# Kernel tuning notes

Hardware: AMD Instinct MI355X
Metric: run time of the kernel (lower is better)

The kernel has to match this reference:

```python
import jax, jax.numpy as jnp
import numpy as np

B, S, D, H = 2, 2048, 1024, 16
DEPTH = D // H

def setup_inputs() -> dict:
    key = jax.random.key(0)
    ks = jax.random.split(key, 6)
    sc = 0.02
    return {
        "x": jax.random.normal(ks[0], (B, S, D), dtype=jnp.float32),
        "mask": jnp.ones((S, S), dtype=jnp.int32),
        "wq": jax.random.normal(ks[1], (D, D), dtype=jnp.float32) * sc,
        "bq": jnp.zeros((D,), dtype=jnp.float32),
        "wk": jax.random.normal(ks[2], (D, D), dtype=jnp.float32) * sc,
        "bk": jnp.zeros((D,), dtype=jnp.float32),
        "wv": jax.random.normal(ks[3], (D, D), dtype=jnp.float32) * sc,
        "bv": jnp.zeros((D,), dtype=jnp.float32),
        "wo": jax.random.normal(ks[4], (D, D), dtype=jnp.float32) * sc,
        "bo": jnp.zeros((D,), dtype=jnp.float32),
    }

def _split_heads(t):
    # [B,S,D] -> [B,H,S,depth]
    b, s, _ = t.shape
    return t.reshape(b, s, H, DEPTH).transpose(0, 2, 1, 3)

def reference(x, mask, wq, bq, wk, bk, wv, bv, wo, bo):
    q = _split_heads(x @ wq + bq)
    k = _split_heads(x @ wk + bk)
    v = _split_heads(x @ wv + bv)
    scale = 1.0 / jnp.sqrt(jnp.asarray(DEPTH, x.dtype))
    scores = jnp.einsum('bhqd,bhkd->bhqk', q, k) * scale
    # Faithful to original: band_part(ones,-1,0) is the LOWER triangle
    # (incl. diagonal), and it is ADDED times -1e9 -> lower triangle masked.
    s_len = mask.shape[0]
    tri = jnp.tril(jnp.ones((s_len, s_len), dtype=x.dtype))
    scores = scores + tri * (-1e9)
    attn = jax.nn.softmax(scores, axis=-1)  # dropout is identity at inference
    out = jnp.einsum('bhqk,bhkd->bhqd', attn, v)
    out = out.transpose(0, 2, 1, 3).reshape(x.shape[0], -1, D)
    return out @ wo + bo
```

## Files before the change

### kernel.cpp

```cpp
#include <hip/hip_runtime.h>
#include <hip/hip_bf16.h>


using bf16   = __bf16;
using bf16x2 = __attribute__((ext_vector_type(2))) __bf16;
using bf16x4 = __attribute__((ext_vector_type(4))) __bf16;
using bf16x8 = __attribute__((ext_vector_type(8))) __bf16;
using f32x4  = __attribute__((ext_vector_type(4))) float;
using uintx2 = __attribute__((ext_vector_type(2))) unsigned int;
using uintx4 = __attribute__((ext_vector_type(4))) unsigned int;

__device__ __forceinline__ void load_lds16(const void* g, void* l) {
  __builtin_amdgcn_global_load_lds(
      (const __attribute__((address_space(1))) void*)g,
      (__attribute__((address_space(3))) void*)l, 16, 0, 0);
}

__device__ __forceinline__ unsigned int packbf(float a, float b) {
  bf16x2 v;
  v[0] = (bf16)a;
  v[1] = (bf16)b;
  return __builtin_bit_cast(unsigned int, v);
}

__device__ __forceinline__ void xchg_p(unsigned int u, unsigned int v, int hi,
                                       unsigned int& f, unsigned int& s) {
#if __has_builtin(__builtin_amdgcn_permlane32_swap) && \
    __has_builtin(__builtin_amdgcn_permlane16_swap)
  uintx2 ab = __builtin_amdgcn_permlane32_swap(u, v, false, false);
  uintx2 fs = __builtin_amdgcn_permlane16_swap(ab[0], ab[1], false, false);
  f = fs[0];
  s = fs[1];
#else
  unsigned int a = (hi < 2) ? u : (unsigned int)__shfl_xor((int)v, 32);
  unsigned int b = (hi < 2) ? (unsigned int)__shfl_xor((int)u, 32) : v;
  unsigned int a16 = (unsigned int)__shfl_xor((int)a, 16);
  unsigned int b16 = (unsigned int)__shfl_xor((int)b, 16);
  f = (hi & 1) ? b16 : a;
  s = (hi & 1) ? b : a16;
#endif
}

__global__ __launch_bounds__(256) void prep_kernel(
    const float* __restrict__ x, bf16* __restrict__ xb,
    const float* __restrict__ wq, const float* __restrict__ wk,
    const float* __restrict__ wv, const float* __restrict__ wo,
    bf16* __restrict__ wT) {
  const int t = threadIdx.x;
  int bid = blockIdx.x;
  if (bid < 4096) {
    const int i = (bid * 256 + t) * 4;
    const float4 v = *(const float4*)(x + i);
    bf16x4 o;
    o[0] = (bf16)v.x; o[1] = (bf16)v.y; o[2] = (bf16)v.z; o[3] = (bf16)v.w;
    *(bf16x4*)(xb + i) = o;
    return;
  }
  bid -= 4096;
  const int sel = bid >> 8;
  const float* w = (sel == 0) ? wq : (sel == 1) ? wk : (sel == 2) ? wv : wo;
  bf16* out = wT + (size_t)sel * 1048576;
  __shared__ float tile[64][65];
  const int n0 = (bid & 15) * 64;
  const int k0 = ((bid >> 4) & 15) * 64;
#pragma unroll
  for (int p = 0; p < 4; ++p) {
    const int row = p * 16 + (t >> 4);
    const int c4  = (t & 15) * 4;
    const float4 v = *(const float4*)&w[(size_t)(k0 + row) * 1024 + n0 + c4];
    tile[row][c4 + 0] = v.x; tile[row][c4 + 1] = v.y;
    tile[row][c4 + 2] = v.z; tile[row][c4 + 3] = v.w;
  }
  __syncthreads();
#pragma unroll
  for (int p = 0; p < 4; ++p) {
    const int rn = p * 16 + (t >> 4);
    const int c4 = (t & 15) * 4;
    bf16x4 o;
#pragma unroll
    for (int j = 0; j < 4; ++j) o[j] = (bf16)tile[c4 + j][rn];
    *(bf16x4*)&out[(size_t)(n0 + rn) * 1024 + k0 + c4] = o;
  }
}

template <int MODE>
__global__ __launch_bounds__(256, 2) void gemm_bt(
    const bf16* __restrict__ A, const bf16* __restrict__ Bt,
    const float* __restrict__ bias0, const float* __restrict__ bias1,
    const float* __restrict__ bias2, bf16* __restrict__ qf,
    bf16* __restrict__ kf, bf16* __restrict__ vt, float* __restrict__ fout,
    int Nblocks) {
  __shared__ __align__(16) char smem[32768];
  char* sA = smem;
  char* sB = smem + 16384;
  const int tid = threadIdx.x;
  const int lane = tid & 63;
  const int w = tid >> 6;
  const int wm = w >> 1, wn = w & 1;
  const int bid = blockIdx.x;
  const int m0 = (bid / Nblocks) * 128;
  const int n0 = (bid % Nblocks) * 128;

  const char* Ab = (const char*)A;
  const char* Bb = (const char*)Bt;
  size_t srcA[4], srcB[4];
#pragma unroll
  for (int it = 0; it < 4; ++it) {
    const int o = it * 4096 + tid * 16;
    const int r = o >> 7;
    const int cg = ((o >> 4) & 7) ^ (r & 7);
    srcA[it] = (size_t)(m0 + r) * 2048 + cg * 16;
    srcB[it] = (size_t)(n0 + r) * 2048 + cg * 16;
  }

  f32x4 acc[4][4] = {};

  for (int kt = 0; kt < 16; ++kt) {
    const size_t kb = (size_t)kt * 128;
#pragma unroll
    for (int it = 0; it < 4; ++it) {
      load_lds16(Ab + srcA[it] + kb, sA + it * 4096 + w * 1024);
      load_lds16(Bb + srcB[it] + kb, sB + it * 4096 + w * 1024);
    }
    asm volatile("s_waitcnt vmcnt(0)" ::: "memory");
    __syncthreads();
#pragma unroll
    for (int ks = 0; ks < 2; ++ks) {
      bf16x8 aF[4], bF[4];
      const int g = (lane >> 4) + 4 * ks;
#pragma unroll
      for (int i = 0; i < 4; ++i) {
        const int ra = wm * 64 + i * 16 + (lane & 15);
        aF[i] = *(const bf16x8*)(sA + ra * 128 + ((g ^ (ra & 7)) << 4));
        const int rb = wn * 64 + i * 16 + (lane & 15);
        bF[i] = *(const bf16x8*)(sB + rb * 128 + ((g ^ (rb & 7)) << 4));
      }
#pragma unroll
      for (int mi = 0; mi < 4; ++mi)
#pragma unroll
        for (int ni = 0; ni < 4; ++ni)
          acc[mi][ni] = __builtin_amdgcn_mfma_f32_16x16x32_bf16(
              aF[mi], bF[ni], acc[mi][ni], 0, 0, 0);
    }
    __syncthreads();
  }

  const int cn = lane & 15;
  const int gq = lane >> 4;
#pragma unroll
  for (int mi = 0; mi < 4; ++mi) {
#pragma unroll
    for (int ni = 0; ni < 4; ++ni) {
      const int n  = n0 + wn * 64 + ni * 16 + cn;
      const int mb = m0 + wm * 64 + mi * 16 + 4 * gq;
      const f32x4 v = acc[mi][ni];
      if (MODE == 0) {
        const float bias =
            (n < 1024) ? bias0[n] : ((n < 2048) ? bias1[n - 1024] : bias2[n - 2048]);
        if (n < 2048) {
          bf16* dst = (n < 1024) ? qf : kf;
          const int nn = n & 1023;
#pragma unroll
          for (int j = 0; j < 4; ++j)
            dst[(size_t)(mb + j) * 1024 + nn] = (bf16)(v[j] + bias);
        } else {
          const int nn = n - 2048;
          const int hh = nn >> 6, dd = nn & 63;
          const int bb = mb >> 11, ss = mb & 2047;
          bf16x4 pk;
#pragma unroll
          for (int j = 0; j < 4; ++j) pk[j] = (bf16)(v[j] + bias);
          *(bf16x4*)(vt + ((size_t)((bb * 16 + hh) * 64 + dd) * 2048 + ss)) = pk;
        }
      } else {
        const float bias = bias0[n];
#pragma unroll
        for (int j = 0; j < 4; ++j)
          fout[(size_t)(mb + j) * 1024 + n] = v[j] + bias;
      }
    }
  }
}

__global__ __launch_bounds__(256, 3) void attn_kernel(
    const bf16* __restrict__ qf, const bf16* __restrict__ kf,
    const bf16* __restrict__ vt, bf16* __restrict__ ao,
    bf16* __restrict__ o2buf, float* __restrict__ mlbuf) {
  __shared__ __align__(16) char smem[32768];

  const unsigned int TAB[24] = {
      0u | (0u << 8)  | (16u << 16) | (1u << 24),
      0u | (16u << 8) | (32u << 16) | (2u << 24),
      1u | (2u << 8)  | (17u << 16) | (1u << 24),
      1u | (17u << 8) | (32u << 16) | (2u << 24),
      2u | (4u << 8)  | (18u << 16) | (1u << 24),
      2u | (18u << 8) | (32u << 16) | (2u << 24),
      3u | (6u << 8)  | (19u << 16) | (1u << 24),
      4u | (8u << 8)  | (20u << 16) | (1u << 24),
      8u | (16u << 8) | (32u << 16) | (0u << 24),
      9u | (18u << 8) | (32u << 16) | (0u << 24),
      3u | (19u << 8) | (32u << 16) | (2u << 24),
      5u | (10u << 8) | (21u << 16) | (1u << 24),
      5u | (21u << 8) | (32u << 16) | (2u << 24),
      6u | (12u << 8) | (22u << 16) | (1u << 24),
      4u | (20u << 8) | (32u << 16) | (2u << 24),
      10u | (20u << 8) | (32u << 16) | (0u << 24),
      15u | (30u << 8) | (32u << 16) | (0u << 24),
      14u | (28u << 8) | (32u << 16) | (0u << 24),
      13u | (26u << 8) | (32u << 16) | (0u << 24),
      12u | (24u << 8) | (32u << 16) | (0u << 24),
      7u | (14u << 8) | (23u << 16) | (1u << 24),
      6u | (22u << 8) | (32u << 16) | (2u << 24),
      7u | (23u << 8) | (32u << 16) | (2u << 24),
      11u | (22u << 8) | (32u << 16) | (0u << 24)};

  const int tid  = threadIdx.x;
  const int lane = tid & 63;
  const int hi   = lane >> 4;
  const int qlo  = lane & 15;
  const int w    = tid >> 6;
  const int u  = blockIdx.x >> 5;
  const int bh = blockIdx.x & 31;
  const int b = bh >> 4, h = bh & 15;
  const unsigned int ent = TAB[u];
  const int jq = ent & 255, kbeg = (ent >> 8) & 255, kend = (ent >> 16) & 255;
  const int mode = ent >> 24;

  const char* kbase = (const char*)kf + ((size_t)b * 2048) * 2048 + h * 128;
  const char* vbase = (const char*)vt + (size_t)bh * 262144;
  const char* qbb   = (const char*)qf + ((size_t)b * 2048) * 2048 + h * 128;

  const int sr  = tid >> 3;
  const int scg = (tid & 7) ^ (sr & 7);

  bf16x8 onesB;
#pragma unroll
  for (int i = 0; i < 8; ++i) onesB[i] = (bf16)1.0f;

  const int q0 = jq * 128;
  const int qb = q0 + w * 32;

  bf16x8 qA[2][2];
#pragma unroll
  for (int nt = 0; nt < 2; ++nt) {
    const char* qrow = qbb + (size_t)(qb + 16 * nt + qlo) * 2048;
#pragma unroll
    for (int ks = 0; ks < 2; ++ks) {
      qA[nt][ks] = *(const bf16x8*)(qrow + ks * 64 + hi * 16);
#pragma unroll
      for (int i = 0; i < 8; ++i)
        qA[nt][ks][i] = (bf16)(0.125f * (float)qA[nt][ks][i]);
    }
  }

  float m[2] = {-1e30f, -1e30f};
  f32x4 lacc[2] = {};
  f32x4 O[2][4] = {};

  auto STAGE = [&](int kt, int bufi) {
    char* dK = smem + bufi * 8192 + w * 1024;
    char* dV = smem + 16384 + bufi * 8192 + w * 1024;
    const int kn = kt * 64;
#pragma unroll
    for (int p = 0; p < 2; ++p) {
      load_lds16(kbase + (size_t)(kn + sr + 32 * p) * 2048 + scg * 16,
                 dK + p * 4096);
      load_lds16(vbase + (size_t)(sr + 32 * p) * 4096 + (size_t)kn * 2 +
                     scg * 16,
                 dV + p * 4096);
    }
  };

  STAGE(kbeg, 0);
  __syncthreads();

  for (int kt = kbeg; kt < kend; ++kt) {
    const int cur = (kt - kbeg) & 1;

    if (kt + 1 < kend) STAGE(kt + 1, cur ^ 1);

    const char* bK = smem + cur * 8192;
    const char* bV = smem + 16384 + cur * 8192;

    f32x4 sc[2][4] = {};
#pragma unroll
    for (int ks = 0; ks < 2; ++ks) {
      const int g = hi + 4 * ks;
#pragma unroll
      for (int t = 0; t < 4; ++t) {
        const int rk = t * 16 + qlo;
        const bf16x8 kF =
            *(const bf16x8*)(bK + rk * 128 + ((g ^ (rk & 7)) << 4));
        sc[0][t] = __builtin_amdgcn_mfma_f32_16x16x32_bf16(kF, qA[0][ks],
                                                           sc[0][t], 0, 0, 0);
        sc[1][t] = __builtin_amdgcn_mfma_f32_16x16x32_bf16(kF, qA[1][ks],
                                                           sc[1][t], 0, 0, 0);
      }
    }

    if (kt * 64 < q0 + 128) {
      const int k0t = kt * 64;
#pragma unroll
      for (int nt = 0; nt < 2; ++nt)
#pragma unroll
        for (int t = 0; t < 4; ++t)
#pragma unroll
          for (int j = 0; j < 4; ++j) {
            const int kk = k0t + t * 16 + 4 * hi + j;
            const int qq = qb + 16 * nt + qlo;
            if (kk <= qq) sc[nt][t][j] = -1e30f;
          }
    }

    float tm[2];
#pragma unroll
    for (int nt = 0; nt < 2; ++nt) {
      float v = sc[nt][0][0];
#pragma unroll
      for (int t = 0; t < 4; ++t)
#pragma unroll
        for (int j = 0; j < 4; ++j) v = fmaxf(v, sc[nt][t][j]);
      v = fmaxf(v, __shfl_xor(v, 16));
      v = fmaxf(v, __shfl_xor(v, 32));
      tm[nt] = v;
    }

    const bool grew = (tm[0] - m[0] > 8.0f) || (tm[1] - m[1] > 8.0f);
    if (__any(grew)) {
#pragma unroll
      for (int nt = 0; nt < 2; ++nt) {
        const float mn = fmaxf(m[nt], tm[nt]);
        const float al = __expf(m[nt] - mn);
        m[nt] = mn;
#pragma unroll
        for (int j = 0; j < 4; ++j) {
          const float alj = __shfl(al, 4 * hi + j);
          lacc[nt][j] *= alj;
#pragma unroll
          for (int dt = 0; dt < 4; ++dt) O[nt][dt][j] *= alj;
        }
      }
    }

    bf16x8 pA[2][2];
#pragma unroll
    for (int nt = 0; nt < 2; ++nt) {
      unsigned int W[4][2];
#pragma unroll
      for (int t = 0; t < 4; ++t)
#pragma unroll
        for (int p = 0; p < 2; ++p)
          W[t][p] = packbf(__expf(sc[nt][t][2 * p] - m[nt]),
                           __expf(sc[nt][t][2 * p + 1] - m[nt]));
#pragma unroll
      for (int ks = 0; ks < 2; ++ks) {
        uintx4 w4;
#pragma unroll
        for (int p = 0; p < 2; ++p) {
          unsigned int f, s;
          xchg_p(W[2 * ks][p], W[2 * ks + 1][p], hi, f, s);
          w4[p] = f;
          w4[2 + p] = s;
        }
        pA[nt][ks] = __builtin_bit_cast(bf16x8, w4);
        lacc[nt] = __builtin_amdgcn_mfma_f32_16x16x32_bf16(pA[nt][ks], onesB,
                                                           lacc[nt], 0, 0, 0);
      }
    }

#pragma unroll
    for (int ks = 0; ks < 2; ++ks) {
      const int g = hi + 4 * ks;
#pragma unroll
      for (int dt = 0; dt < 4; ++dt) {
        const int rv = dt * 16 + qlo;
        const bf16x8 vF =
            *(const bf16x8*)(bV + rv * 128 + ((g ^ (rv & 7)) << 4));
        O[0][dt] = __builtin_amdgcn_mfma_f32_16x16x32_bf16(pA[0][ks], vF,
                                                           O[0][dt], 0, 0, 0);
        O[1][dt] = __builtin_amdgcn_mfma_f32_16x16x32_bf16(pA[1][ks], vF,
                                                           O[1][dt], 0, 0, 0);
      }
    }
    __syncthreads();
  }

  if (mode == 0) {
#pragma unroll
    for (int nt = 0; nt < 2; ++nt)
#pragma unroll
      for (int j = 0; j < 4; ++j) {
        const float linv = (lacc[nt][j] > 0.f) ? 1.f / lacc[nt][j] : 0.f;
        const int qg = qb + 16 * nt + 4 * hi + j;
#pragma unroll
        for (int dt = 0; dt < 4; ++dt)
          ao[(size_t)(b * 2048 + qg) * 1024 + h * 64 + dt * 16 + qlo] =
              (bf16)(O[nt][dt][j] * linv);
      }
  } else {
    const int qtbh = jq * 32 + bh;
    const int slot = mode - 1;
#pragma unroll
    for (int nt = 0; nt < 2; ++nt)
#pragma unroll
      for (int j = 0; j < 4; ++j) {
        const int r = w * 32 + 16 * nt + 4 * hi + j;
#pragma unroll
        for (int dt = 0; dt < 4; ++dt) {
          const bf16 vv = (bf16)O[nt][dt][j];
          if (mode == 1)
            ao[(size_t)(b * 2048 + q0 + r) * 1024 + h * 64 + dt * 16 + qlo] = vv;
          else
            o2buf[(size_t)(qtbh * 128 + r) * 64 + dt * 16 + qlo] = vv;
        }
      }
    if (qlo == 0) {
#pragma unroll
      for (int nt = 0; nt < 2; ++nt)
#pragma unroll
        for (int j = 0; j < 4; ++j)
          mlbuf[((qtbh * 2 + slot) * 2 + 1) * 128 + (w * 32 + 16 * nt + 4 * hi + j)] =
              lacc[nt][j];
    }
    if (hi == 0) {
#pragma unroll
      for (int nt = 0; nt < 2; ++nt)
        mlbuf[((qtbh * 2 + slot) * 2 + 0) * 128 + (w * 32 + 16 * nt + qlo)] =
            m[nt];
    }
  }
}

__global__ __launch_bounds__(256) void combine_kernel(
    const bf16* __restrict__ o2buf, const float* __restrict__ mlbuf,
    bf16* __restrict__ ao) {
  const int qtbh = blockIdx.x;
  const int jq = qtbh >> 5, bh = qtbh & 31;
  const int b = bh >> 4, h = bh & 15;
  const int t = threadIdx.x;
  const int r = t >> 1;
  const int c0 = (t & 1) * 32;

  const float m1 = mlbuf[((qtbh * 2 + 0) * 2 + 0) * 128 + r];
  const float l1 = mlbuf[((qtbh * 2 + 0) * 2 + 1) * 128 + r];
  const float m2 = mlbuf[((qtbh * 2 + 1) * 2 + 0) * 128 + r];
  const float l2 = mlbuf[((qtbh * 2 + 1) * 2 + 1) * 128 + r];
  const float M  = fmaxf(m1, m2);
  const float w1 = __expf(m1 - M), w2 = __expf(m2 - M);
  const float denom = w1 * l1 + w2 * l2;
  const float linv = (denom > 0.f) ? 1.f / denom : 0.f;

  bf16* arow = ao + ((size_t)(b * 2048 + jq * 128 + r) * 1024 + h * 64 + c0);
  const bf16* o2row = o2buf + ((size_t)(qtbh * 128 + r) * 64 + c0);
#pragma unroll
  for (int i = 0; i < 4; ++i) {
    const bf16x8 o1 = *(const bf16x8*)(arow + i * 8);
    const bf16x8 o2 = *(const bf16x8*)(o2row + i * 8);
    bf16x8 o;
#pragma unroll
    for (int j = 0; j < 8; ++j)
      o[j] = (bf16)((w1 * (float)o1[j] + w2 * (float)o2[j]) * linv);
    *(bf16x8*)(arow + i * 8) = o;
  }
}

__global__ __launch_bounds__(256) void vmean_kernel(const bf16* __restrict__ vt,
                                                    bf16* __restrict__ ao) {
  const int tid = threadIdx.x;
  const int lane = tid & 63, w = tid >> 6;
  const int gw = blockIdx.x * 4 + w;
  const int bh = gw >> 6, d = gw & 63;
  const int b = bh >> 4, h = bh & 15;
  const bf16x8* p = (const bf16x8*)(vt + (size_t)gw * 2048 + lane * 32);
  float s = 0.f;
#pragma unroll
  for (int i = 0; i < 4; ++i) {
    const bf16x8 v = p[i];
#pragma unroll
    for (int j = 0; j < 8; ++j) s += (float)v[j];
  }
  for (int off = 1; off < 64; off <<= 1) s += __shfl_xor(s, off);
  if (lane == 0)
    ao[(size_t)(b * 2048 + 2047) * 1024 + h * 64 + d] = (bf16)(s * (1.f / 2048.f));
}

extern "C" void kernel_launch(void* const* d_in, const int* in_sizes, int n_in,
                              void* d_out, int out_size, void* d_ws,
                              size_t ws_size, hipStream_t stream) {
  const float* x  = (const float*)d_in[0];
  const float* wq = (const float*)d_in[2];
  const float* bq = (const float*)d_in[3];
  const float* wk = (const float*)d_in[4];
  const float* bk = (const float*)d_in[5];
  const float* wv = (const float*)d_in[6];
  const float* bv = (const float*)d_in[7];
  const float* wo = (const float*)d_in[8];
  const float* bo = (const float*)d_in[9];
  float* out = (float*)d_out;

  if (ws_size < (size_t)25165824 * 2) return;

  bf16* ws    = (bf16*)d_ws;
  bf16* xb    = ws;
  bf16* wqkvT = xb + 4194304;
  bf16* woT   = wqkvT + 3145728;
  bf16* qfp   = woT + 1048576;
  bf16* kfp   = qfp + 4194304;
  bf16* vtp   = kfp + 4194304;
  bf16* aop   = vtp + 4194304;

  bf16*  o2buf = xb;
  float* mlbuf = (float*)(xb + 2097152);

  prep_kernel<<<5120, 256, 0, stream>>>(x, xb, wq, wk, wv, wo, wqkvT);

  gemm_bt<0><<<32 * 24, 256, 0, stream>>>(xb, wqkvT, bq, bk, bv, qfp, kfp, vtp,
                                          nullptr, 24);
  attn_kernel<<<768, 256, 0, stream>>>(qfp, kfp, vtp, aop, o2buf, mlbuf);
  vmean_kernel<<<512, 256, 0, stream>>>(vtp, aop);
  combine_kernel<<<256, 256, 0, stream>>>(o2buf, mlbuf, aop);
  gemm_bt<1><<<32 * 8, 256, 0, stream>>>(aop, woT, bo, nullptr, nullptr, nullptr,
                                         nullptr, nullptr, out, 8);
}
```

Baseline: 106.9 us.

## Make attention kernel persistent with atomic work-queue scheduling

The attention kernel becomes persistent: 512 blocks repeatedly take work units from a global atomic counter that prep_kernel resets, and the unit table moves to device constant memory in a new order. The goal is to balance the uneven causal-split work across CUs dynamically instead of relying on the hardware's static block dispatch. Launch bounds drop from 3 to 2 waves per EU to match the persistent grid. This adds one atomic plus a block barrier per unit and uses fewer resident blocks, so some latency hiding may be lost.

```diff
diff --git a/kernel.cpp b/kernel.cpp
--- a/kernel.cpp
+++ b/kernel.cpp
@@ -9,6 +9,32 @@
 using f32x4  = __attribute__((ext_vector_type(4))) float;
 using uintx2 = __attribute__((ext_vector_type(2))) unsigned int;
 using uintx4 = __attribute__((ext_vector_type(4))) unsigned int;
+
+__device__ const unsigned int kUnitTab[24] = {
+    0u | (0u << 8)  | (16u << 16) | (1u << 24),
+    0u | (16u << 8) | (32u << 16) | (2u << 24),
+    8u | (16u << 8) | (32u << 16) | (0u << 24),
+    1u | (2u << 8)  | (17u << 16) | (1u << 24),
+    1u | (17u << 8) | (32u << 16) | (2u << 24),
+    2u | (4u << 8)  | (18u << 16) | (1u << 24),
+    2u | (18u << 8) | (32u << 16) | (2u << 24),
+    9u | (18u << 8) | (32u << 16) | (0u << 24),
+    3u | (6u << 8)  | (19u << 16) | (1u << 24),
+    3u | (19u << 8) | (32u << 16) | (2u << 24),
+    4u | (8u << 8)  | (20u << 16) | (1u << 24),
+    4u | (20u << 8) | (32u << 16) | (2u << 24),
+    10u | (20u << 8) | (32u << 16) | (0u << 24),
+    5u | (10u << 8) | (21u << 16) | (1u << 24),
+    5u | (21u << 8) | (32u << 16) | (2u << 24),
+    6u | (12u << 8) | (22u << 16) | (1u << 24),
+    6u | (22u << 8) | (32u << 16) | (2u << 24),
+    11u | (22u << 8) | (32u << 16) | (0u << 24),
+    7u | (14u << 8) | (23u << 16) | (1u << 24),
+    7u | (23u << 8) | (32u << 16) | (2u << 24),
+    12u | (24u << 8) | (32u << 16) | (0u << 24),
+    13u | (26u << 8) | (32u << 16) | (0u << 24),
+    14u | (28u << 8) | (32u << 16) | (0u << 24),
+    15u | (30u << 8) | (32u << 16) | (0u << 24)};
 
 __device__ __forceinline__ void load_lds16(const void* g, void* l) {
   __builtin_amdgcn_global_load_lds(
@@ -45,9 +71,10 @@
     const float* __restrict__ x, bf16* __restrict__ xb,
     const float* __restrict__ wq, const float* __restrict__ wk,
     const float* __restrict__ wv, const float* __restrict__ wo,
-    bf16* __restrict__ wT) {
+    bf16* __restrict__ wT, int* __restrict__ ctr) {
   const int t = threadIdx.x;
   int bid = blockIdx.x;
+  if (bid == 0 && t == 0) *ctr = 0;
   if (bid < 4096) {
     const int i = (bid * 256 + t) * 4;
     const float4 v = *(const float4*)(x + i);
@@ -182,53 +209,19 @@
   }
 }
 
-__global__ __launch_bounds__(256, 3) void attn_kernel(
+__global__ __launch_bounds__(256, 2) void attn_kernel(
     const bf16* __restrict__ qf, const bf16* __restrict__ kf,
     const bf16* __restrict__ vt, bf16* __restrict__ ao,
-    bf16* __restrict__ o2buf, float* __restrict__ mlbuf) {
+    bf16* __restrict__ o2buf, float* __restrict__ mlbuf,
+    int* __restrict__ ctr) {
   __shared__ __align__(16) char smem[32768];
-
-  const unsigned int TAB[24] = {
-      0u | (0u << 8)  | (16u << 16) | (1u << 24),
-      0u | (16u << 8) | (32u << 16) | (2u << 24),
-      1u | (2u << 8)  | (17u << 16) | (1u << 24),
-      1u | (17u << 8) | (32u << 16) | (2u << 24),
-      2u | (4u << 8)  | (18u << 16) | (1u << 24),
-      2u | (18u << 8) | (32u << 16) | (2u << 24),
-      3u | (6u << 8)  | (19u << 16) | (1u << 24),
-      4u | (8u << 8)  | (20u << 16) | (1u << 24),
-      8u | (16u << 8) | (32u << 16) | (0u << 24),
-      9u | (18u << 8) | (32u << 16) | (0u << 24),
-      3u | (19u << 8) | (32u << 16) | (2u << 24),
-      5u | (10u << 8) | (21u << 16) | (1u << 24),
-      5u | (21u << 8) | (32u << 16) | (2u << 24),
-      6u | (12u << 8) | (22u << 16) | (1u << 24),
-      4u | (20u << 8) | (32u << 16) | (2u << 24),
-      10u | (20u << 8) | (32u << 16) | (0u << 24),
-      15u | (30u << 8) | (32u << 16) | (0u << 24),
-      14u | (28u << 8) | (32u << 16) | (0u << 24),
-      13u | (26u << 8) | (32u << 16) | (0u << 24),
-      12u | (24u << 8) | (32u << 16) | (0u << 24),
-      7u | (14u << 8) | (23u << 16) | (1u << 24),
-      6u | (22u << 8) | (32u << 16) | (2u << 24),
-      7u | (23u << 8) | (32u << 16) | (2u << 24),
-      11u | (22u << 8) | (32u << 16) | (0u << 24)};
+  __shared__ int s_g;
 
   const int tid  = threadIdx.x;
   const int lane = tid & 63;
   const int hi   = lane >> 4;
   const int qlo  = lane & 15;
   const int w    = tid >> 6;
-  const int u  = blockIdx.x >> 5;
-  const int bh = blockIdx.x & 31;
-  const int b = bh >> 4, h = bh & 15;
-  const unsigned int ent = TAB[u];
-  const int jq = ent & 255, kbeg = (ent >> 8) & 255, kend = (ent >> 16) & 255;
-  const int mode = ent >> 24;
-
-  const char* kbase = (const char*)kf + ((size_t)b * 2048) * 2048 + h * 128;
-  const char* vbase = (const char*)vt + (size_t)bh * 262144;
-  const char* qbb   = (const char*)qf + ((size_t)b * 2048) * 2048 + h * 128;
 
   const int sr  = tid >> 3;
   const int scg = (tid & 7) ^ (sr & 7);
@@ -237,196 +230,215 @@
 #pragma unroll
   for (int i = 0; i < 8; ++i) onesB[i] = (bf16)1.0f;
 
-  const int q0 = jq * 128;
-  const int qb = q0 + w * 32;
-
-  bf16x8 qA[2][2];
-#pragma unroll
-  for (int nt = 0; nt < 2; ++nt) {
-    const char* qrow = qbb + (size_t)(qb + 16 * nt + qlo) * 2048;
-#pragma unroll
-    for (int ks = 0; ks < 2; ++ks) {
-      qA[nt][ks] = *(const bf16x8*)(qrow + ks * 64 + hi * 16);
-#pragma unroll
-      for (int i = 0; i < 8; ++i)
-        qA[nt][ks][i] = (bf16)(0.125f * (float)qA[nt][ks][i]);
+  for (;;) {
+    if (tid == 0) s_g = atomicAdd(ctr, 1);
+    __syncthreads();
+    const int g = s_g;
+    if (g >= 768) break;
+
+    const unsigned int ent = kUnitTab[g >> 5];
+    const int bh = g & 31;
+    const int b = bh >> 4, h = bh & 15;
+    const int jq = ent & 255, kbeg = (ent >> 8) & 255,
+              kend = (ent >> 16) & 255;
+    const int mode = ent >> 24;
+
+    const char* kbase = (const char*)kf + ((size_t)b * 2048) * 2048 + h * 128;
+    const char* vbase = (const char*)vt + (size_t)bh * 262144;
+    const char* qbb   = (const char*)qf + ((size_t)b * 2048) * 2048 + h * 128;
+
+    const int q0 = jq * 128;
+    const int qb = q0 + w * 32;
+
+    bf16x8 qA[2][2];
+#pragma unroll
+    for (int nt = 0; nt < 2; ++nt) {
+      const char* qrow = qbb + (size_t)(qb + 16 * nt + qlo) * 2048;
+#pragma unroll
+      for (int ks = 0; ks < 2; ++ks) {
+        qA[nt][ks] = *(const bf16x8*)(qrow + ks * 64 + hi * 16);
+#pragma unroll
+        for (int i = 0; i < 8; ++i)
+          qA[nt][ks][i] = (bf16)(0.125f * (float)qA[nt][ks][i]);
+      }
     }
-  }
-
-  float m[2] = {-1e30f, -1e30f};
-  f32x4 lacc[2] = {};
-  f32x4 O[2][4] = {};
-
-  auto STAGE = [&](int kt, int bufi) {
-    char* dK = smem + bufi * 8192 + w * 1024;
-    char* dV = smem + 16384 + bufi * 8192 + w * 1024;
-    const int kn = kt * 64;
-#pragma unroll
-    for (int p = 0; p < 2; ++p) {
-      load_lds16(kbase + (size_t)(kn + sr + 32 * p) * 2048 + scg * 16,
-                 dK + p * 4096);
-      load_lds16(vbase + (size_t)(sr + 32 * p) * 4096 + (size_t)kn * 2 +
-                     scg * 16,
-                 dV + p * 4096);
+
+    float m[2] = {-1e30f, -1e30f};
+    f32x4 lacc[2] = {};
+    f32x4 O[2][4] = {};
+
+    auto STAGE = [&](int kt, int bufi) {
+      char* dK = smem + bufi * 8192 + w * 1024;
+      char* dV = smem + 16384 + bufi * 8192 + w * 1024;
+      const int kn = kt * 64;
+#pragma unroll
+      for (int p = 0; p < 2; ++p) {
+        load_lds16(kbase + (size_t)(kn + sr + 32 * p) * 2048 + scg * 16,
+                   dK + p * 4096);
+        load_lds16(vbase + (size_t)(sr + 32 * p) * 4096 + (size_t)kn * 2 +
+                       scg * 16,
+                   dV + p * 4096);
+      }
+    };
+
+    STAGE(kbeg, 0);
+    __syncthreads();
+
+    for (int kt = kbeg; kt < kend; ++kt) {
+      const int cur = (kt - kbeg) & 1;
+
+      if (kt + 1 < kend) STAGE(kt + 1, cur ^ 1);
+
+      const char* bK = smem + cur * 8192;
+      const char* bV = smem + 16384 + cur * 8192;
+
+      f32x4 sc[2][4] = {};
+#pragma unroll
+      for (int ks = 0; ks < 2; ++ks) {
+        const int gg = hi + 4 * ks;
+#pragma unroll
+        for (int t = 0; t < 4; ++t) {
+          const int rk = t * 16 + qlo;
+          const bf16x8 kF =
+              *(const bf16x8*)(bK + rk * 128 + ((gg ^ (rk & 7)) << 4));
+          sc[0][t] = __builtin_amdgcn_mfma_f32_16x16x32_bf16(kF, qA[0][ks],
+                                                             sc[0][t], 0, 0, 0);
+          sc[1][t] = __builtin_amdgcn_mfma_f32_16x16x32_bf16(kF, qA[1][ks],
+                                                             sc[1][t], 0, 0, 0);
+        }
+      }
+
+      if (kt * 64 < q0 + 128) {
+        const int k0t = kt * 64;
+#pragma unroll
+        for (int nt = 0; nt < 2; ++nt)
+#pragma unroll
+          for (int t = 0; t < 4; ++t)
+#pragma unroll
+            for (int j = 0; j < 4; ++j) {
+              const int kk = k0t + t * 16 + 4 * hi + j;
+              const int qq = qb + 16 * nt + qlo;
+              if (kk <= qq) sc[nt][t][j] = -1e30f;
+            }
+      }
+
+      float tm[2];
+#pragma unroll
+      for (int nt = 0; nt < 2; ++nt) {
+        float v = sc[nt][0][0];
+#pragma unroll
+        for (int t = 0; t < 4; ++t)
+#pragma unroll
+          for (int j = 0; j < 4; ++j) v = fmaxf(v, sc[nt][t][j]);
+        v = fmaxf(v, __shfl_xor(v, 16));
+        v = fmaxf(v, __shfl_xor(v, 32));
+        tm[nt] = v;
+      }
+
+      const bool grew = (tm[0] - m[0] > 8.0f) || (tm[1] - m[1] > 8.0f);
+      if (__any(grew)) {
+#pragma unroll
+        for (int nt = 0; nt < 2; ++nt) {
+          const float mn = fmaxf(m[nt], tm[nt]);
+          const float al = __expf(m[nt] - mn);
+          m[nt] = mn;
+#pragma unroll
+          for (int j = 0; j < 4; ++j) {
+            const float alj = __shfl(al, 4 * hi + j);
+            lacc[nt][j] *= alj;
+#pragma unroll
+            for (int dt = 0; dt < 4; ++dt) O[nt][dt][j] *= alj;
+          }
+        }
+      }
+
+      bf16x8 pA[2][2];
+#pragma unroll
+      for (int nt = 0; nt < 2; ++nt) {
+        unsigned int W[4][2];
+#pragma unroll
+        for (int t = 0; t < 4; ++t)
+#pragma unroll
+          for (int p = 0; p < 2; ++p)
+            W[t][p] = packbf(__expf(sc[nt][t][2 * p] - m[nt]),
+                             __expf(sc[nt][t][2 * p + 1] - m[nt]));
+#pragma unroll
+        for (int ks = 0; ks < 2; ++ks) {
+          uintx4 w4;
+#pragma unroll
+          for (int p = 0; p < 2; ++p) {
+            unsigned int f, s;
+            xchg_p(W[2 * ks][p], W[2 * ks + 1][p], hi, f, s);
+            w4[p] = f;
+            w4[2 + p] = s;
+          }
+          pA[nt][ks] = __builtin_bit_cast(bf16x8, w4);
+          lacc[nt] = __builtin_amdgcn_mfma_f32_16x16x32_bf16(pA[nt][ks], onesB,
+                                                             lacc[nt], 0, 0, 0);
+        }
+      }
+
+#pragma unroll
+      for (int ks = 0; ks < 2; ++ks) {
+        const int gg = hi + 4 * ks;
+#pragma unroll
+        for (int dt = 0; dt < 4; ++dt) {
+          const int rv = dt * 16 + qlo;
+          const bf16x8 vF =
+              *(const bf16x8*)(bV + rv * 128 + ((gg ^ (rv & 7)) << 4));
+          O[0][dt] = __builtin_amdgcn_mfma_f32_16x16x32_bf16(pA[0][ks], vF,
+                                                             O[0][dt], 0, 0, 0);
+          O[1][dt] = __builtin_amdgcn_mfma_f32_16x16x32_bf16(pA[1][ks], vF,
+                                                             O[1][dt], 0, 0, 0);
+        }
+      }
+      __syncthreads();
     }
-  };
-
-  STAGE(kbeg, 0);
-  __syncthreads();
-
-  for (int kt = kbeg; kt < kend; ++kt) {
-    const int cur = (kt - kbeg) & 1;
-
-    if (kt + 1 < kend) STAGE(kt + 1, cur ^ 1);
-
-    const char* bK = smem + cur * 8192;
-    const char* bV = smem + 16384 + cur * 8192;
-
-    f32x4 sc[2][4] = {};
-#pragma unroll
-    for (int ks = 0; ks < 2; ++ks) {
-      const int g = hi + 4 * ks;
-#pragma unroll
-      for (int t = 0; t < 4; ++t) {
-        const int rk = t * 16 + qlo;
-        const bf16x8 kF =
-            *(const bf16x8*)(bK + rk * 128 + ((g ^ (rk & 7)) << 4));
-        sc[0][t] = __builtin_amdgcn_mfma_f32_16x16x32_bf16(kF, qA[0][ks],
-                                                           sc[0][t], 0, 0, 0);
-        sc[1][t] = __builtin_amdgcn_mfma_f32_16x16x32_bf16(kF, qA[1][ks],
-                                                           sc[1][t], 0, 0, 0);
-      }
-    }
-
-    if (kt * 64 < q0 + 128) {
-      const int k0t = kt * 64;
+
+    if (mode == 0) {
 #pragma unroll
       for (int nt = 0; nt < 2; ++nt)
 #pragma unroll
-        for (int t = 0; t < 4; ++t)
-#pragma unroll
-          for (int j = 0; j < 4; ++j) {
-            const int kk = k0t + t * 16 + 4 * hi + j;
-            const int qq = qb + 16 * nt + qlo;
-            if (kk <= qq) sc[nt][t][j] = -1e30f;
+        for (int j = 0; j < 4; ++j) {
+          const float linv = (lacc[nt][j] > 0.f) ? 1.f / lacc[nt][j] : 0.f;
+          const int qg = qb + 16 * nt + 4 * hi + j;
+#pragma unroll
+          for (int dt = 0; dt < 4; ++dt)
+            ao[(size_t)(b * 2048 + qg) * 1024 + h * 64 + dt * 16 + qlo] =
+                (bf16)(O[nt][dt][j] * linv);
+        }
+    } else {
+      const int qtbh = jq * 32 + bh;
+      const int slot = mode - 1;
+#pragma unroll
+      for (int nt = 0; nt < 2; ++nt)
+#pragma unroll
+        for (int j = 0; j < 4; ++j) {
+          const int r = w * 32 + 16 * nt + 4 * hi + j;
+#pragma unroll
+          for (int dt = 0; dt < 4; ++dt) {
+            const bf16 vv = (bf16)O[nt][dt][j];
+            if (mode == 1)
+              ao[(size_t)(b * 2048 + q0 + r) * 1024 + h * 64 + dt * 16 + qlo] =
+                  vv;
+            else
+              o2buf[(size_t)(qtbh * 128 + r) * 64 + dt * 16 + qlo] = vv;
           }
-    }
-
-    float tm[2];
-#pragma unroll
-    for (int nt = 0; nt < 2; ++nt) {
-      float v = sc[nt][0][0];
-#pragma unroll
-      for (int t = 0; t < 4; ++t)
-#pragma unroll
-        for (int j = 0; j < 4; ++j) v = fmaxf(v, sc[nt][t][j]);
-      v = fmaxf(v, __shfl_xor(v, 16));
-      v = fmaxf(v, __shfl_xor(v, 32));
-      tm[nt] = v;
-    }
-
-    const bool grew = (tm[0] - m[0] > 8.0f) || (tm[1] - m[1] > 8.0f);
-    if (__any(grew)) {
-#pragma unroll
-      for (int nt = 0; nt < 2; ++nt) {
-        const float mn = fmaxf(m[nt], tm[nt]);
-        const float al = __expf(m[nt] - mn);
-        m[nt] = mn;
-#pragma unroll
-        for (int j = 0; j < 4; ++j) {
-          const float alj = __shfl(al, 4 * hi + j);
-          lacc[nt][j] *= alj;
-#pragma unroll
-          for (int dt = 0; dt < 4; ++dt) O[nt][dt][j] *= alj;
-        }
-      }
-    }
-
-    bf16x8 pA[2][2];
-#pragma unroll
-    for (int nt = 0; nt < 2; ++nt) {
-      unsigned int W[4][2];
-#pragma unroll
-      for (int t = 0; t < 4; ++t)
-#pragma unroll
-        for (int p = 0; p < 2; ++p)
-          W[t][p] = packbf(__expf(sc[nt][t][2 * p] - m[nt]),
-                           __expf(sc[nt][t][2 * p + 1] - m[nt]));
-#pragma unroll
-      for (int ks = 0; ks < 2; ++ks) {
-        uintx4 w4;
-#pragma unroll
-        for (int p = 0; p < 2; ++p) {
-          unsigned int f, s;
-          xchg_p(W[2 * ks][p], W[2 * ks + 1][p], hi, f, s);
-          w4[p] = f;
-          w4[2 + p] = s;
-        }
-        pA[nt][ks] = __builtin_bit_cast(bf16x8, w4);
-        lacc[nt] = __builtin_amdgcn_mfma_f32_16x16x32_bf16(pA[nt][ks], onesB,
-                                                           lacc[nt], 0, 0, 0);
-      }
-    }
-
-#pragma unroll
-    for (int ks = 0; ks < 2; ++ks) {
-      const int g = hi + 4 * ks;
-#pragma unroll
-      for (int dt = 0; dt < 4; ++dt) {
-        const int rv = dt * 16 + qlo;
-        const bf16x8 vF =
-            *(const bf16x8*)(bV + rv * 128 + ((g ^ (rv & 7)) << 4));
-        O[0][dt] = __builtin_amdgcn_mfma_f32_16x16x32_bf16(pA[0][ks], vF,
-                                                           O[0][dt], 0, 0, 0);
-        O[1][dt] = __builtin_amdgcn_mfma_f32_16x16x32_bf16(pA[1][ks], vF,
-                                                           O[1][dt], 0, 0, 0);
-      }
-    }
-    __syncthreads();
-  }
-
-  if (mode == 0) {
-#pragma unroll
-    for (int nt = 0; nt < 2; ++nt)
-#pragma unroll
-      for (int j = 0; j < 4; ++j) {
-        const float linv = (lacc[nt][j] > 0.f) ? 1.f / lacc[nt][j] : 0.f;
-        const int qg = qb + 16 * nt + 4 * hi + j;
-#pragma unroll
-        for (int dt = 0; dt < 4; ++dt)
-          ao[(size_t)(b * 2048 + qg) * 1024 + h * 64 + dt * 16 + qlo] =
-              (bf16)(O[nt][dt][j] * linv);
-      }
-  } else {
-    const int qtbh = jq * 32 + bh;
-    const int slot = mode - 1;
-#pragma unroll
-    for (int nt = 0; nt < 2; ++nt)
-#pragma unroll
-      for (int j = 0; j < 4; ++j) {
-        const int r = w * 32 + 16 * nt + 4 * hi + j;
-#pragma unroll
-        for (int dt = 0; dt < 4; ++dt) {
-          const bf16 vv = (bf16)O[nt][dt][j];
-          if (mode == 1)
-            ao[(size_t)(b * 2048 + q0 + r) * 1024 + h * 64 + dt * 16 + qlo] = vv;
-          else
-            o2buf[(size_t)(qtbh * 128 + r) * 64 + dt * 16 + qlo] = vv;
-        }
-      }
-    if (qlo == 0) {
-#pragma unroll
-      for (int nt = 0; nt < 2; ++nt)
-#pragma unroll
-        for (int j = 0; j < 4; ++j)
-          mlbuf[((qtbh * 2 + slot) * 2 + 1) * 128 + (w * 32 + 16 * nt + 4 * hi + j)] =
-              lacc[nt][j];
-    }
-    if (hi == 0) {
-#pragma unroll
-      for (int nt = 0; nt < 2; ++nt)
-        mlbuf[((qtbh * 2 + slot) * 2 + 0) * 128 + (w * 32 + 16 * nt + qlo)] =
-            m[nt];
+        }
+      if (qlo == 0) {
+#pragma unroll
+        for (int nt = 0; nt < 2; ++nt)
+#pragma unroll
+          for (int j = 0; j < 4; ++j)
+            mlbuf[((qtbh * 2 + slot) * 2 + 1) * 128 +
+                  (w * 32 + 16 * nt + 4 * hi + j)] = lacc[nt][j];
+      }
+      if (hi == 0) {
+#pragma unroll
+        for (int nt = 0; nt < 2; ++nt)
+          mlbuf[((qtbh * 2 + slot) * 2 + 0) * 128 + (w * 32 + 16 * nt + qlo)] =
+              m[nt];
+      }
     }
   }
 }
@@ -498,7 +510,7 @@
   const float* bo = (const float*)d_in[9];
   float* out = (float*)d_out;
 
-  if (ws_size < (size_t)25165824 * 2) return;
+  if (ws_size < (size_t)25165824 * 2 + 64) return;
 
   bf16* ws    = (bf16*)d_ws;
   bf16* xb    = ws;
@@ -508,15 +520,16 @@
   bf16* kfp   = qfp + 4194304;
   bf16* vtp   = kfp + 4194304;
   bf16* aop   = vtp + 4194304;
+  int*  ctr   = (int*)(aop + 4194304);
 
   bf16*  o2buf = xb;
   float* mlbuf = (float*)(xb + 2097152);
 
-  prep_kernel<<<5120, 256, 0, stream>>>(x, xb, wq, wk, wv, wo, wqkvT);
+  prep_kernel<<<5120, 256, 0, stream>>>(x, xb, wq, wk, wv, wo, wqkvT, ctr);
 
   gemm_bt<0><<<32 * 24, 256, 0, stream>>>(xb, wqkvT, bq, bk, bv, qfp, kfp, vtp,
                                           nullptr, 24);
-  attn_kernel<<<768, 256, 0, stream>>>(qfp, kfp, vtp, aop, o2buf, mlbuf);
+  attn_kernel<<<512, 256, 0, stream>>>(qfp, kfp, vtp, aop, o2buf, mlbuf, ctr);
   vmean_kernel<<<512, 256, 0, stream>>>(vtp, aop);
   combine_kernel<<<256, 256, 0, stream>>>(o2buf, mlbuf, aop);
   gemm_bt<1><<<32 * 8, 256, 0, stream>>>(aop, woT, bo, nullptr, nullptr, nullptr,
```

After: 121.1 us. +13.3%, slower.

## Pair causal attention segments per block to balance work across 512 blocks

Applied to the files above, without the earlier changes.

Replaces the 24-entry work table with a computed schedule. Blocks 0-7 each handle one long first-half segment. Blocks 8-15 each run two segments back to back, pairing query tile j's tail with query tile 15-j so every block covers about 15-16 key tiles. The grid shrinks from 768 to 512 blocks and the launch-bounds occupancy hint drops from 3 to 2. The aim is evenly sized blocks in a single wave, cutting tail imbalance and per-block launch overhead, at the cost of less parallelism and a serial second segment that reloads Q and restarts the pipeline.

```diff
diff --git a/kernel.cpp b/kernel.cpp
--- a/kernel.cpp
+++ b/kernel.cpp
@@ -182,37 +182,11 @@
   }
 }
 
-__global__ __launch_bounds__(256, 3) void attn_kernel(
+__global__ __launch_bounds__(256, 2) void attn_kernel(
     const bf16* __restrict__ qf, const bf16* __restrict__ kf,
     const bf16* __restrict__ vt, bf16* __restrict__ ao,
     bf16* __restrict__ o2buf, float* __restrict__ mlbuf) {
   __shared__ __align__(16) char smem[32768];
-
-  const unsigned int TAB[24] = {
-      0u | (0u << 8)  | (16u << 16) | (1u << 24),
-      0u | (16u << 8) | (32u << 16) | (2u << 24),
-      1u | (2u << 8)  | (17u << 16) | (1u << 24),
-      1u | (17u << 8) | (32u << 16) | (2u << 24),
-      2u | (4u << 8)  | (18u << 16) | (1u << 24),
-      2u | (18u << 8) | (32u << 16) | (2u << 24),
-      3u | (6u << 8)  | (19u << 16) | (1u << 24),
-      4u | (8u << 8)  | (20u << 16) | (1u << 24),
-      8u | (16u << 8) | (32u << 16) | (0u << 24),
-      9u | (18u << 8) | (32u << 16) | (0u << 24),
-      3u | (19u << 8) | (32u << 16) | (2u << 24),
-      5u | (10u << 8) | (21u << 16) | (1u << 24),
-      5u | (21u << 8) | (32u << 16) | (2u << 24),
-      6u | (12u << 8) | (22u << 16) | (1u << 24),
-      4u | (20u << 8) | (32u << 16) | (2u << 24),
-      10u | (20u << 8) | (32u << 16) | (0u << 24),
-      15u | (30u << 8) | (32u << 16) | (0u << 24),
-      14u | (28u << 8) | (32u << 16) | (0u << 24),
-      13u | (26u << 8) | (32u << 16) | (0u << 24),
-      12u | (24u << 8) | (32u << 16) | (0u << 24),
-      7u | (14u << 8) | (23u << 16) | (1u << 24),
-      6u | (22u << 8) | (32u << 16) | (2u << 24),
-      7u | (23u << 8) | (32u << 16) | (2u << 24),
-      11u | (22u << 8) | (32u << 16) | (0u << 24)};
 
   const int tid  = threadIdx.x;
   const int lane = tid & 63;
@@ -222,9 +196,6 @@
   const int u  = blockIdx.x >> 5;
   const int bh = blockIdx.x & 31;
   const int b = bh >> 4, h = bh & 15;
-  const unsigned int ent = TAB[u];
-  const int jq = ent & 255, kbeg = (ent >> 8) & 255, kend = (ent >> 16) & 255;
-  const int mode = ent >> 24;
 
   const char* kbase = (const char*)kf + ((size_t)b * 2048) * 2048 + h * 128;
   const char* vbase = (const char*)vt + (size_t)bh * 262144;
@@ -237,197 +208,216 @@
 #pragma unroll
   for (int i = 0; i < 8; ++i) onesB[i] = (bf16)1.0f;
 
-  const int q0 = jq * 128;
-  const int qb = q0 + w * 32;
-
-  bf16x8 qA[2][2];
-#pragma unroll
-  for (int nt = 0; nt < 2; ++nt) {
-    const char* qrow = qbb + (size_t)(qb + 16 * nt + qlo) * 2048;
-#pragma unroll
-    for (int ks = 0; ks < 2; ++ks) {
-      qA[nt][ks] = *(const bf16x8*)(qrow + ks * 64 + hi * 16);
-#pragma unroll
-      for (int i = 0; i < 8; ++i)
-        qA[nt][ks][i] = (bf16)(0.125f * (float)qA[nt][ks][i]);
+  int nseg, sjq[2], skb[2], ske[2], smode[2];
+  if (u < 8) {
+    nseg = 1;
+    sjq[0] = u; skb[0] = 2 * u; ske[0] = 2 * u + 17; smode[0] = 1;
+    sjq[1] = 0; skb[1] = 0; ske[1] = 0; smode[1] = 0;
+  } else {
+    const int j = u - 8;
+    nseg = 2;
+    sjq[0] = j;      skb[0] = 2 * j + 17; ske[0] = 32; smode[0] = 2;
+    sjq[1] = 15 - j; skb[1] = 30 - 2 * j; ske[1] = 32; smode[1] = 0;
+  }
+
+  for (int seg = 0; seg < nseg; ++seg) {
+    const int jq = sjq[seg], kbeg = skb[seg], kend = ske[seg];
+    const int mode = smode[seg];
+
+    const int q0 = jq * 128;
+    const int qb = q0 + w * 32;
+
+    bf16x8 qA[2][2];
+#pragma unroll
+    for (int nt = 0; nt < 2; ++nt) {
+      const char* qrow = qbb + (size_t)(qb + 16 * nt + qlo) * 2048;
+#pragma unroll
+      for (int ks = 0; ks < 2; ++ks) {
+        qA[nt][ks] = *(const bf16x8*)(qrow + ks * 64 + hi * 16);
+#pragma unroll
+        for (int i = 0; i < 8; ++i)
+          qA[nt][ks][i] = (bf16)(0.125f * (float)qA[nt][ks][i]);
+      }
     }
-  }
-
-  float m[2] = {-1e30f, -1e30f};
-  f32x4 lacc[2] = {};
-  f32x4 O[2][4] = {};
-
-  auto STAGE = [&](int kt, int bufi) {
-    char* dK = smem + bufi * 8192 + w * 1024;
-    char* dV = smem + 16384 + bufi * 8192 + w * 1024;
-    const int kn = kt * 64;
-#pragma unroll
-    for (int p = 0; p < 2; ++p) {
-      load_lds16(kbase + (size_t)(kn + sr + 32 * p) * 2048 + scg * 16,
-                 dK + p * 4096);
-      load_lds16(vbase + (size_t)(sr + 32 * p) * 4096 + (size_t)kn * 2 +
-                     scg * 16,
-                 dV + p * 4096);
+
+    float m[2] = {-1e30f, -1e30f};
+    f32x4 lacc[2] = {};
+    f32x4 O[2][4] = {};
+
+    auto STAGE = [&](int kt, int bufi) {
+      char* dK = smem + bufi * 8192 + w * 1024;
+      char* dV = smem + 16384 + bufi * 8192 + w * 1024;
+      const int kn = kt * 64;
+#pragma unroll
+      for (int p = 0; p < 2; ++p) {
+        load_lds16(kbase + (size_t)(kn + sr + 32 * p) * 2048 + scg * 16,
+                   dK + p * 4096);
+        load_lds16(vbase + (size_t)(sr + 32 * p) * 4096 + (size_t)kn * 2 +
+                       scg * 16,
+                   dV + p * 4096);
+      }
+    };
+
+    STAGE(kbeg, 0);
+    __syncthreads();
+
+    for (int kt = kbeg; kt < kend; ++kt) {
+      const int cur = (kt - kbeg) & 1;
+
+      if (kt + 1 < kend) STAGE(kt + 1, cur ^ 1);
+
+      const char* bK = smem + cur * 8192;
+      const char* bV = smem + 16384 + cur * 8192;
+
+      f32x4 sc[2][4] = {};
+#pragma unroll
+      for (int ks = 0; ks < 2; ++ks) {
+        const int gg = hi + 4 * ks;
+#pragma unroll
+        for (int t = 0; t < 4; ++t) {
+          const int rk = t * 16 + qlo;
+          const bf16x8 kF =
+              *(const bf16x8*)(bK + rk * 128 + ((gg ^ (rk & 7)) << 4));
+          sc[0][t] = __builtin_amdgcn_mfma_f32_16x16x32_bf16(kF, qA[0][ks],
+                                                             sc[0][t], 0, 0, 0);
+          sc[1][t] = __builtin_amdgcn_mfma_f32_16x16x32_bf16(kF, qA[1][ks],
+                                                             sc[1][t], 0, 0, 0);
+        }
+      }
+
+      if (kt * 64 < q0 + 128) {
+        const int k0t = kt * 64;
+#pragma unroll
+        for (int nt = 0; nt < 2; ++nt)
+#pragma unroll
+          for (int t = 0; t < 4; ++t)
+#pragma unroll
+            for (int j = 0; j < 4; ++j) {
+              const int kk = k0t + t * 16 + 4 * hi + j;
+              const int qq = qb + 16 * nt + qlo;
+              if (kk <= qq) sc[nt][t][j] = -1e30f;
+            }
+      }
+
+      float tm[2];
+#pragma unroll
+      for (int nt = 0; nt < 2; ++nt) {
+        float v = sc[nt][0][0];
+#pragma unroll
+        for (int t = 0; t < 4; ++t)
+#pragma unroll
+          for (int j = 0; j < 4; ++j) v = fmaxf(v, sc[nt][t][j]);
+        v = fmaxf(v, __shfl_xor(v, 16));
+        v = fmaxf(v, __shfl_xor(v, 32));
+        tm[nt] = v;
+      }
+
+      const bool grew = (tm[0] - m[0] > 8.0f) || (tm[1] - m[1] > 8.0f);
+      if (__any(grew)) {
+#pragma unroll
+        for (int nt = 0; nt < 2; ++nt) {
+          const float mn = fmaxf(m[nt], tm[nt]);
+          const float al = __expf(m[nt] - mn);
+          m[nt] = mn;
+#pragma unroll
+          for (int j = 0; j < 4; ++j) {
+            const float alj = __shfl(al, 4 * hi + j);
+            lacc[nt][j] *= alj;
+#pragma unroll
+            for (int dt = 0; dt < 4; ++dt) O[nt][dt][j] *= alj;
+          }
+        }
+      }
+
+      bf16x8 pA[2][2];
+#pragma unroll
+      for (int nt = 0; nt < 2; ++nt) {
+        unsigned int W[4][2];
+#pragma unroll
+        for (int t = 0; t < 4; ++t)
+#pragma unroll
+          for (int p = 0; p < 2; ++p)
+            W[t][p] = packbf(__expf(sc[nt][t][2 * p] - m[nt]),
+                             __expf(sc[nt][t][2 * p + 1] - m[nt]));
+#pragma unroll
+        for (int ks = 0; ks < 2; ++ks) {
+          uintx4 w4;
+#pragma unroll
+          for (int p = 0; p < 2; ++p) {
+            unsigned int f, s;
+            xchg_p(W[2 * ks][p], W[2 * ks + 1][p], hi, f, s);
+            w4[p] = f;
+            w4[2 + p] = s;
+          }
+          pA[nt][ks] = __builtin_bit_cast(bf16x8, w4);
+          lacc[nt] = __builtin_amdgcn_mfma_f32_16x16x32_bf16(pA[nt][ks], onesB,
+                                                             lacc[nt], 0, 0, 0);
+        }
+      }
+
+#pragma unroll
+      for (int ks = 0; ks < 2; ++ks) {
+        const int gg = hi + 4 * ks;
+#pragma unroll
+        for (int dt = 0; dt < 4; ++dt) {
+          const int rv = dt * 16 + qlo;
+          const bf16x8 vF =
+              *(const bf16x8*)(bV + rv * 128 + ((gg ^ (rv & 7)) << 4));
+          O[0][dt] = __builtin_amdgcn_mfma_f32_16x16x32_bf16(pA[0][ks], vF,
+                                                             O[0][dt], 0, 0, 0);
+          O[1][dt] = __builtin_amdgcn_mfma_f32_16x16x32_bf16(pA[1][ks], vF,
+                                                             O[1][dt], 0, 0, 0);
+        }
+      }
+      __syncthreads();
     }
-  };
-
-  STAGE(kbeg, 0);
-  __syncthreads();
-
-  for (int kt = kbeg; kt < kend; ++kt) {
-    const int cur = (kt - kbeg) & 1;
-
-    if (kt + 1 < kend) STAGE(kt + 1, cur ^ 1);
-
-    const char* bK = smem + cur * 8192;
-    const char* bV = smem + 16384 + cur * 8192;
-
-    f32x4 sc[2][4] = {};
-#pragma unroll
-    for (int ks = 0; ks < 2; ++ks) {
-      const int g = hi + 4 * ks;
-#pragma unroll
-      for (int t = 0; t < 4; ++t) {
-        const int rk = t * 16 + qlo;
-        const bf16x8 kF =
-            *(const bf16x8*)(bK + rk * 128 + ((g ^ (rk & 7)) << 4));
-        sc[0][t] = __builtin_amdgcn_mfma_f32_16x16x32_bf16(kF, qA[0][ks],
-                                                           sc[0][t], 0, 0, 0);
-        sc[1][t] = __builtin_amdgcn_mfma_f32_16x16x32_bf16(kF, qA[1][ks],
-                                                           sc[1][t], 0, 0, 0);
-      }
-    }
-
-    if (kt * 64 < q0 + 128) {
-      const int k0t = kt * 64;
+
+    if (mode == 0) {
 #pragma unroll
       for (int nt = 0; nt < 2; ++nt)
 #pragma unroll
-        for (int t = 0; t < 4; ++t)
-#pragma unroll
-          for (int j = 0; j < 4; ++j) {
-            const int kk = k0t + t * 16 + 4 * hi + j;
-            const int qq = qb + 16 * nt + qlo;
-            if (kk <= qq) sc[nt][t][j] = -1e30f;
+        for (int j = 0; j < 4; ++j) {
+          const float linv = (lacc[nt][j] > 0.f) ? 1.f / lacc[nt][j] : 0.f;
+          const int qg = qb + 16 * nt + 4 * hi + j;
+#pragma unroll
+          for (int dt = 0; dt < 4; ++dt)
+            ao[(size_t)(b * 2048 + qg) * 1024 + h * 64 + dt * 16 + qlo] =
+                (bf16)(O[nt][dt][j] * linv);
+        }
+    } else {
+      const int qtbh = jq * 32 + bh;
+      const int slot = mode - 1;
+#pragma unroll
+      for (int nt = 0; nt < 2; ++nt)
+#pragma unroll
+        for (int j = 0; j < 4; ++j) {
+          const int r = w * 32 + 16 * nt + 4 * hi + j;
+#pragma unroll
+          for (int dt = 0; dt < 4; ++dt) {
+            const bf16 vv = (bf16)O[nt][dt][j];
+            if (mode == 1)
+              ao[(size_t)(b * 2048 + q0 + r) * 1024 + h * 64 + dt * 16 + qlo] =
+                  vv;
+            else
+              o2buf[(size_t)(qtbh * 128 + r) * 64 + dt * 16 + qlo] = vv;
           }
-    }
-
-    float tm[2];
-#pragma unroll
-    for (int nt = 0; nt < 2; ++nt) {
-      float v = sc[nt][0][0];
-#pragma unroll
-      for (int t = 0; t < 4; ++t)
-#pragma unroll
-        for (int j = 0; j < 4; ++j) v = fmaxf(v, sc[nt][t][j]);
-      v = fmaxf(v, __shfl_xor(v, 16));
-      v = fmaxf(v, __shfl_xor(v, 32));
-      tm[nt] = v;
-    }
-
-    const bool grew = (tm[0] - m[0] > 8.0f) || (tm[1] - m[1] > 8.0f);
-    if (__any(grew)) {
-#pragma unroll
-      for (int nt = 0; nt < 2; ++nt) {
-        const float mn = fmaxf(m[nt], tm[nt]);
-        const float al = __expf(m[nt] - mn);
-        m[nt] = mn;
-#pragma unroll
-        for (int j = 0; j < 4; ++j) {
-          const float alj = __shfl(al, 4 * hi + j);
-          lacc[nt][j] *= alj;
-#pragma unroll
-          for (int dt = 0; dt < 4; ++dt) O[nt][dt][j] *= alj;
-        }
-      }
-    }
-
-    bf16x8 pA[2][2];
-#pragma unroll
-    for (int nt = 0; nt < 2; ++nt) {
-      unsigned int W[4][2];
-#pragma unroll
-      for (int t = 0; t < 4; ++t)
-#pragma unroll
-        for (int p = 0; p < 2; ++p)
-          W[t][p] = packbf(__expf(sc[nt][t][2 * p] - m[nt]),
-                           __expf(sc[nt][t][2 * p + 1] - m[nt]));
-#pragma unroll
-      for (int ks = 0; ks < 2; ++ks) {
-        uintx4 w4;
-#pragma unroll
-        for (int p = 0; p < 2; ++p) {
-          unsigned int f, s;
-          xchg_p(W[2 * ks][p], W[2 * ks + 1][p], hi, f, s);
-          w4[p] = f;
-          w4[2 + p] = s;
-        }
-        pA[nt][ks] = __builtin_bit_cast(bf16x8, w4);
-        lacc[nt] = __builtin_amdgcn_mfma_f32_16x16x32_bf16(pA[nt][ks], onesB,
-                                                           lacc[nt], 0, 0, 0);
-      }
-    }
-
-#pragma unroll
-    for (int ks = 0; ks < 2; ++ks) {
-      const int g = hi + 4 * ks;
-#pragma unroll
-      for (int dt = 0; dt < 4; ++dt) {
-        const int rv = dt * 16 + qlo;
-        const bf16x8 vF =
-            *(const bf16x8*)(bV + rv * 128 + ((g ^ (rv & 7)) << 4));
-        O[0][dt] = __builtin_amdgcn_mfma_f32_16x16x32_bf16(pA[0][ks], vF,
-                                                           O[0][dt], 0, 0, 0);
-        O[1][dt] = __builtin_amdgcn_mfma_f32_16x16x32_bf16(pA[1][ks], vF,
-                                                           O[1][dt], 0, 0, 0);
+        }
+      if (qlo == 0) {
+#pragma unroll
+        for (int nt = 0; nt < 2; ++nt)
+#pragma unroll
+          for (int j = 0; j < 4; ++j)
+            mlbuf[((qtbh * 2 + slot) * 2 + 1) * 128 +
+                  (w * 32 + 16 * nt + 4 * hi + j)] = lacc[nt][j];
+      }
+      if (hi == 0) {
+#pragma unroll
+        for (int nt = 0; nt < 2; ++nt)
+          mlbuf[((qtbh * 2 + slot) * 2 + 0) * 128 + (w * 32 + 16 * nt + qlo)] =
+              m[nt];
       }
     }
     __syncthreads();
-  }
-
-  if (mode == 0) {
-#pragma unroll
-    for (int nt = 0; nt < 2; ++nt)
-#pragma unroll
-      for (int j = 0; j < 4; ++j) {
-        const float linv = (lacc[nt][j] > 0.f) ? 1.f / lacc[nt][j] : 0.f;
-        const int qg = qb + 16 * nt + 4 * hi + j;
-#pragma unroll
-        for (int dt = 0; dt < 4; ++dt)
-          ao[(size_t)(b * 2048 + qg) * 1024 + h * 64 + dt * 16 + qlo] =
-              (bf16)(O[nt][dt][j] * linv);
-      }
-  } else {
-    const int qtbh = jq * 32 + bh;
-    const int slot = mode - 1;
-#pragma unroll
-    for (int nt = 0; nt < 2; ++nt)
-#pragma unroll
-      for (int j = 0; j < 4; ++j) {
-        const int r = w * 32 + 16 * nt + 4 * hi + j;
-#pragma unroll
-        for (int dt = 0; dt < 4; ++dt) {
-          const bf16 vv = (bf16)O[nt][dt][j];
-          if (mode == 1)
-            ao[(size_t)(b * 2048 + q0 + r) * 1024 + h * 64 + dt * 16 + qlo] = vv;
-          else
-            o2buf[(size_t)(qtbh * 128 + r) * 64 + dt * 16 + qlo] = vv;
-        }
-      }
-    if (qlo == 0) {
-#pragma unroll
-      for (int nt = 0; nt < 2; ++nt)
-#pragma unroll
-        for (int j = 0; j < 4; ++j)
-          mlbuf[((qtbh * 2 + slot) * 2 + 1) * 128 + (w * 32 + 16 * nt + 4 * hi + j)] =
-              lacc[nt][j];
-    }
-    if (hi == 0) {
-#pragma unroll
-      for (int nt = 0; nt < 2; ++nt)
-        mlbuf[((qtbh * 2 + slot) * 2 + 0) * 128 + (w * 32 + 16 * nt + qlo)] =
-            m[nt];
-    }
   }
 }
 
@@ -516,7 +506,7 @@
 
   gemm_bt<0><<<32 * 24, 256, 0, stream>>>(xb, wqkvT, bq, bk, bv, qfp, kfp, vtp,
                                           nullptr, 24);
-  attn_kernel<<<768, 256, 0, stream>>>(qfp, kfp, vtp, aop, o2buf, mlbuf);
+  attn_kernel<<<512, 256, 0, stream>>>(qfp, kfp, vtp, aop, o2buf, mlbuf);
   vmean_kernel<<<512, 256, 0, stream>>>(vtp, aop);
   combine_kernel<<<256, 256, 0, stream>>>(o2buf, mlbuf, aop);
   gemm_bt<1><<<32 * 8, 256, 0, stream>>>(aop, woT, bo, nullptr, nullptr, nullptr,
```

Result: no change. 108.0 us (+1.0%).
